# Performance work log

Measured on AMD Instinct MI355X. Metric: run time of the kernel, lower is better.

## Reference

```python
import jax, jax.numpy as jnp
import numpy as np

EMB_SIZE = 256  # VQ embedding_size
BETA = 0.25     # commitment cost


def _mlp(x, W1, b1, W2, b2, W3, b3):
    h = jax.nn.relu(x @ W1 + b1)
    h = jax.nn.relu(h @ W2 + b2)
    return h @ W3 + b3


def setup_inputs() -> dict:
    key = jax.random.key(0)
    ks = jax.random.split(key, 5)
    B, D = 1024, 1024
    s = 1.0 / np.sqrt(D)
    return {
        "observation": jax.random.normal(ks[0], (B, D), jnp.float32),
        "W1": jax.random.normal(ks[1], (D, D), jnp.float32) * s,
        "b1": jnp.zeros((D,), jnp.float32),
        "W2": jax.random.normal(ks[2], (D, D), jnp.float32) * s,
        "b2": jnp.zeros((D,), jnp.float32),
        "W3": jax.random.normal(ks[3], (D, D), jnp.float32) * s,
        "b3": jnp.zeros((D,), jnp.float32),
        "codebook": jax.random.normal(ks[4], (512, EMB_SIZE), jnp.float32),
    }


def reference(observation, W1, b1, W2, b2, W3, b3, codebook):
    # Dense encoder
    features = _mlp(observation, W1, b1, W2, b2, W3, b3)  # [B, 1024]
    # Flatten features into embedding_size-dim tokens: [B*4, 256]
    z = features.reshape(-1, EMB_SIZE)
    # Squared euclidean distances to codebook: [N, K]
    d = (jnp.sum(z * z, axis=1, keepdims=True)
         - 2.0 * (z @ codebook.T)
         + jnp.sum(codebook * codebook, axis=1)[None, :])
    idx = jnp.argmin(d, axis=1)                   # [N] nearest code indices
    quantized = codebook[idx]                     # [N, 256] gather
    # VQ losses
    commitment_loss = jnp.mean((jax.lax.stop_gradient(quantized) - z) ** 2)
    codebook_loss = jnp.mean((quantized - jax.lax.stop_gradient(z)) ** 2)
    loss = codebook_loss + BETA * commitment_loss
    # Straight-through estimator
    quantized_st = z + jax.lax.stop_gradient(quantized - z)
    out = quantized_st.reshape(features.shape)    # [B, 1024]
    return out, loss, idx
```

## Files before the change

### kernel.cpp

```cpp
#include <hip/hip_runtime.h>


typedef _Float16 half8 __attribute__((ext_vector_type(8)));
typedef _Float16 half4 __attribute__((ext_vector_type(4)));
typedef float floatx4 __attribute__((ext_vector_type(4)));

#define LO_SCALE 2048.0f
#define INV_LO_SCALE (1.0f / 2048.0f)

__device__ __forceinline__ int remap4(int k0)
{
    return (k0 & 32) | ((k0 & 12) << 1) | ((k0 & 16) >> 2);
}
__device__ __forceinline__ int remap1(int k)
{
    return (k & ~63) | (k & 32) | ((k & 12) << 1) | ((k & 16) >> 2) | (k & 3);
}

__device__ __forceinline__ void gl_lds16(const _Float16* g, _Float16* l)
{
    __builtin_amdgcn_global_load_lds(
        (const __attribute__((address_space(1))) void*)g,
        (__attribute__((address_space(3))) void*)l, 16, 0, 0);
}

__device__ __forceinline__ half8 rfrag(const _Float16* m, int row, int ks, int fg)
{
    const int ch = ((ks << 2) + fg) ^ (row & 7);
    return *reinterpret_cast<const half8*>(&m[(row << 6) + (ch << 3)]);
}

template <bool RELU, bool WF32, bool WSPLIT>
__global__ __launch_bounds__(256) void gemm_k(
    const _Float16* __restrict__ Ah, const _Float16* __restrict__ Al,
    const _Float16* __restrict__ Bh, const _Float16* __restrict__ Bl,
    const float* __restrict__ bias,
    float* __restrict__ Cf, _Float16* __restrict__ Ch, _Float16* __restrict__ Cl,
    int N, int K)
{
    __shared__ __align__(16) _Float16 sm[2][192 * 64];

    const int tid = threadIdx.x;
    const int m0 = blockIdx.y * 32, n0 = blockIdx.x * 64;
    const int w = tid >> 6, lane = tid & 63;
    const int srow = lane >> 3, sc = lane & 7;

    const int wm = (w & 1) * 16, wn = (w >> 1) * 32;
    const int fr = lane & 15, fg = lane >> 4;

    floatx4 hh[2] = {};
    floatx4 m1[2] = {};
    floatx4 m2[2] = {};

    const int NT = K >> 6;

    auto STAGE = [&](int buf, int t) {
        const int kb = t << 6;
        #pragma unroll
        for (int s = 0; s < 6; ++s) {
            const int task = w * 6 + s;
            const _Float16* gb;
            int grow, lrow;
            if (task < 4)       { gb = Ah; grow = m0 + task * 8;        lrow = task * 8; }
            else if (task < 8)  { gb = Al; grow = m0 + (task - 4) * 8;  lrow = 32 + (task - 4) * 8; }
            else if (task < 16) { gb = Bh; grow = n0 + (task - 8) * 8;  lrow = 64 + (task - 8) * 8; }
            else                { gb = Bl; grow = n0 + (task - 16) * 8; lrow = 128 + (task - 16) * 8; }
            const _Float16* g = gb + (size_t)(grow + srow) * K + kb + ((sc ^ srow) << 3);
            gl_lds16(g, &sm[buf][lrow << 6]);
        }
    };

    STAGE(0, 0);
    __syncthreads();

    for (int t = 0; t < NT; ++t) {
        const int cur = t & 1;
        if (t + 1 < NT) STAGE(cur ^ 1, t + 1);
        const _Float16* S0 = sm[cur];
        #pragma unroll
        for (int ks = 0; ks < 2; ++ks) {
            const half8 a_h  = rfrag(S0, wm + fr, ks, fg);
            const half8 a_l  = rfrag(S0, 32 + wm + fr, ks, fg);
            const half8 b_h0 = rfrag(S0, 64 + wn + fr, ks, fg);
            const half8 b_h1 = rfrag(S0, 64 + wn + 16 + fr, ks, fg);
            const half8 b_l0 = rfrag(S0, 128 + wn + fr, ks, fg);
            const half8 b_l1 = rfrag(S0, 128 + wn + 16 + fr, ks, fg);
            hh[0] = __builtin_amdgcn_mfma_f32_16x16x32_f16(a_h, b_h0, hh[0], 0, 0, 0);
            hh[1] = __builtin_amdgcn_mfma_f32_16x16x32_f16(a_h, b_h1, hh[1], 0, 0, 0);
            m1[0] = __builtin_amdgcn_mfma_f32_16x16x32_f16(a_h, b_l0, m1[0], 0, 0, 0);
            m1[1] = __builtin_amdgcn_mfma_f32_16x16x32_f16(a_h, b_l1, m1[1], 0, 0, 0);
            m2[0] = __builtin_amdgcn_mfma_f32_16x16x32_f16(a_l, b_h0, m2[0], 0, 0, 0);
            m2[1] = __builtin_amdgcn_mfma_f32_16x16x32_f16(a_l, b_h1, m2[1], 0, 0, 0);
        }
        __syncthreads();
    }

    #pragma unroll
    for (int j = 0; j < 2; ++j) {
        const int col = n0 + wn + j * 16 + fr;
        const float bv = bias ? bias[col] : 0.0f;
        const int colr = remap1(col);
        #pragma unroll
        for (int r = 0; r < 4; ++r) {
            const int row = m0 + wm + fg * 4 + r;
            float v = hh[j][r] + (m1[j][r] + m2[j][r]) * INV_LO_SCALE + bv;
            if (RELU) v = fmaxf(v, 0.0f);
            if (WF32) Cf[(size_t)row * N + col] = v;
            if (WSPLIT) {
                const size_t o = (size_t)row * N + colr;
                const _Float16 hi = (_Float16)v;
                Ch[o] = hi;
                Cl[o] = (_Float16)((v - (float)hi) * LO_SCALE);
            }
        }
    }
}

__global__ __launch_bounds__(256) void prep_kernel(
    const float* __restrict__ W1, const float* __restrict__ W2,
    const float* __restrict__ W3, const float* __restrict__ obs,
    const float* __restrict__ CB,
    _Float16* __restrict__ T1h, _Float16* __restrict__ T1l,
    _Float16* __restrict__ T2h, _Float16* __restrict__ T2l,
    _Float16* __restrict__ T3h, _Float16* __restrict__ T3l,
    _Float16* __restrict__ Oh, _Float16* __restrict__ Ol,
    _Float16* __restrict__ CBh, _Float16* __restrict__ CBl,
    float* __restrict__ cnorm)
{
    __shared__ float tile[64][65];
    const int b = blockIdx.x, tid = threadIdx.x;

    if (b < 768) {
        const int z = b >> 8, rem = b & 255;
        const float* Wm = (z == 0) ? W1 : (z == 1) ? W2 : W3;
        _Float16* Th = (z == 0) ? T1h : (z == 1) ? T2h : T3h;
        _Float16* Tl = (z == 0) ? T1l : (z == 1) ? T2l : T3l;
        const int nb = (rem & 15) * 64, kb = (rem >> 4) * 64;
        {
            const int kr = tid >> 2, c0 = (tid & 3) * 16;
            #pragma unroll
            for (int c = 0; c < 16; c += 4) {
                float4 v = *reinterpret_cast<const float4*>(
                    &Wm[(size_t)(kb + kr) * 1024 + nb + c0 + c]);
                tile[kr][c0 + c] = v.x; tile[kr][c0 + c + 1] = v.y;
                tile[kr][c0 + c + 2] = v.z; tile[kr][c0 + c + 3] = v.w;
            }
        }
        __syncthreads();
        {
            const int nr = tid >> 2, k0 = (tid & 3) * 16;
            #pragma unroll
            for (int g = 0; g < 4; ++g) {
                const int kk = k0 + g * 4;
                half4 h, lo;
                #pragma unroll
                for (int j = 0; j < 4; ++j) {
                    const float x = tile[kk + j][nr];
                    const _Float16 hi = (_Float16)x;
                    h[j] = hi;
                    lo[j] = (_Float16)((x - (float)hi) * LO_SCALE);
                }
                const size_t o = (size_t)(nb + nr) * 1024 + kb + remap4(kk);
                *reinterpret_cast<half4*>(&Th[o]) = h;
                *reinterpret_cast<half4*>(&Tl[o]) = lo;
            }
        }
    } else if (b < 1280) {
        const size_t e0 = ((size_t)(b - 768) * 256 + tid) * 8;
        float4 a = *reinterpret_cast<const float4*>(&obs[e0]);
        float4 c = *reinterpret_cast<const float4*>(&obs[e0 + 4]);
        float xs[8] = {a.x, a.y, a.z, a.w, c.x, c.y, c.z, c.w};
        half4 h[2], lo[2];
        #pragma unroll
        for (int q = 0; q < 2; ++q)
            #pragma unroll
            for (int j = 0; j < 4; ++j) {
                const float x = xs[q * 4 + j];
                const _Float16 hi = (_Float16)x;
                h[q][j] = hi;
                lo[q][j] = (_Float16)((x - (float)hi) * LO_SCALE);
            }
        const size_t base = e0 & ~(size_t)63;
        const int r1 = remap4((int)(e0 & 63));
        const int r2 = remap4((int)((e0 + 4) & 63));
        *reinterpret_cast<half4*>(&Oh[base + r1]) = h[0];
        *reinterpret_cast<half4*>(&Oh[base + r2]) = h[1];
        *reinterpret_cast<half4*>(&Ol[base + r1]) = lo[0];
        *reinterpret_cast<half4*>(&Ol[base + r2]) = lo[1];
    } else {
        const int wv = tid >> 6, lane = tid & 63;
        const int code = (b - 1280) * 4 + wv;
        const int k0 = lane * 4;
        float4 c = *reinterpret_cast<const float4*>(&CB[(size_t)code * 256 + k0]);
        float xs[4] = {c.x, c.y, c.z, c.w};
        half4 h, lo;
        float s = 0.f;
        #pragma unroll
        for (int j = 0; j < 4; ++j) {
            const _Float16 hi = (_Float16)xs[j];
            h[j] = hi;
            lo[j] = (_Float16)((xs[j] - (float)hi) * LO_SCALE);
            s += xs[j] * xs[j];
        }
        const size_t o = (size_t)code * 256 + (k0 & ~63) + remap4(k0 & 63);
        *reinterpret_cast<half4*>(&CBh[o]) = h;
        *reinterpret_cast<half4*>(&CBl[o]) = lo;
        #pragma unroll
        for (int off = 32; off; off >>= 1) s += __shfl_down(s, off);
        if (lane == 0) cnorm[code] = s;
    }
}

__global__ __launch_bounds__(512) void vq_kernel(
    const _Float16* __restrict__ Fh, const _Float16* __restrict__ Fl,
    const float* __restrict__ S, const float* __restrict__ CB,
    const float* __restrict__ cnorm,
    float* __restrict__ out, float* __restrict__ pl, float* __restrict__ idx_out)
{
    const int wid = threadIdx.x >> 6, lane = threadIdx.x & 63;
    const int n = blockIdx.x * 8 + wid;

    float best = 3.4e38f;
    int bidx = 0x7fffffff;
    #pragma unroll
    for (int j = 0; j < 8; ++j) {
        const int k = j * 64 + lane;
        const float v = fmaf(-2.0f, S[(size_t)n * 512 + k], cnorm[k]);
        if (v < best) { best = v; bidx = k; }
    }
    #pragma unroll
    for (int off = 32; off; off >>= 1) {
        const float ov = __shfl_down(best, off);
        const int oi = __shfl_down(bidx, off);
        if (ov < best || (ov == best && oi < bidx)) { best = ov; bidx = oi; }
    }
    bidx = __shfl(bidx, 0);
    best = __shfl(best, 0);

    const int base = n * 256 + lane * 4;
    half4 h4 = *reinterpret_cast<const half4*>(&Fh[base]);
    half4 l4 = *reinterpret_cast<const half4*>(&Fl[base]);
    float zn = 0.f;
    #pragma unroll
    for (int j = 0; j < 4; ++j) {
        const float z = (float)h4[j] + (float)l4[j] * INV_LO_SCALE;
        zn = fmaf(z, z, zn);
    }
    #pragma unroll
    for (int off = 32; off; off >>= 1) zn += __shfl_down(zn, off);

    float4 q4 = *reinterpret_cast<const float4*>(&CB[(size_t)bidx * 256 + lane * 4]);
    *reinterpret_cast<float4*>(&out[(size_t)n * 256 + lane * 4]) = q4;

    __shared__ float part[8];
    if (lane == 0) {
        part[wid] = zn + best;
        idx_out[n] = (float)bidx;
    }
    __syncthreads();
    if (threadIdx.x == 0) {
        float s = 0.f;
        #pragma unroll
        for (int i = 0; i < 8; ++i) s += part[i];
        pl[blockIdx.x] = s;
    }
}

__global__ __launch_bounds__(512) void finalize_kernel(
    const float* __restrict__ pl, float* __restrict__ loss_out)
{
    float s = pl[threadIdx.x];
    #pragma unroll
    for (int off = 32; off; off >>= 1) s += __shfl_down(s, off);
    __shared__ float p[8];
    if ((threadIdx.x & 63) == 0) p[threadIdx.x >> 6] = s;
    __syncthreads();
    if (threadIdx.x == 0) {
        float t = 0.f;
        #pragma unroll
        for (int i = 0; i < 8; ++i) t += p[i];
        loss_out[0] = 1.25f * t / 1048576.0f;
    }
}

extern "C" void kernel_launch(void* const* d_in, const int* in_sizes, int n_in,
                              void* d_out, int out_size, void* d_ws, size_t ws_size,
                              hipStream_t stream)
{
    const float* obs = (const float*)d_in[0];
    const float* W1  = (const float*)d_in[1];
    const float* b1  = (const float*)d_in[2];
    const float* W2  = (const float*)d_in[3];
    const float* b2  = (const float*)d_in[4];
    const float* W3  = (const float*)d_in[5];
    const float* b3  = (const float*)d_in[6];
    const float* CB  = (const float*)d_in[7];

    float* out = (float*)d_out;
    float* loss_out = out + 1048576;
    float* idx_out  = out + 1048577;

    char* Wp = (char*)d_ws;
    _Float16* Oh    = (_Float16*)(Wp + (0u  << 20));
    _Float16* Ol    = (_Float16*)(Wp + (2u  << 20));
    _Float16* W1t_h = (_Float16*)(Wp + (4u  << 20));
    _Float16* W1t_l = (_Float16*)(Wp + (6u  << 20));
    _Float16* W2t_h = (_Float16*)(Wp + (8u  << 20));
    _Float16* W2t_l = (_Float16*)(Wp + (10u << 20));
    _Float16* W3t_h = (_Float16*)(Wp + (12u << 20));
    _Float16* W3t_l = (_Float16*)(Wp + (14u << 20));
    _Float16* H1_h  = (_Float16*)(Wp + (16u << 20));
    _Float16* H1_l  = (_Float16*)(Wp + (18u << 20));
    _Float16* H2_h  = (_Float16*)(Wp + (20u << 20));
    _Float16* H2_l  = (_Float16*)(Wp + (22u << 20));
    _Float16* F_h   = (_Float16*)(Wp + (24u << 20));
    _Float16* F_l   = (_Float16*)(Wp + (26u << 20));
    float*    S     = (float*)(Wp + (28u << 20));
    _Float16* CB_h  = (_Float16*)(Wp + (36u << 20));
    _Float16* CB_l  = (_Float16*)(Wp + (36u << 20) + 512 * 256 * 2);
    float*    cn    = (float*)(Wp + (36u << 20) + 2 * 512 * 256 * 2);
    float*    pl    = cn + 512;

    prep_kernel<<<1408, 256, 0, stream>>>(
        W1, W2, W3, obs, CB,
        W1t_h, W1t_l, W2t_h, W2t_l, W3t_h, W3t_l,
        Oh, Ol, CB_h, CB_l, cn);

    gemm_k<true, false, true><<<dim3(16, 32), 256, 0, stream>>>(
        Oh, Ol, W1t_h, W1t_l, b1, nullptr, H1_h, H1_l, 1024, 1024);
    gemm_k<true, false, true><<<dim3(16, 32), 256, 0, stream>>>(
        H1_h, H1_l, W2t_h, W2t_l, b2, nullptr, H2_h, H2_l, 1024, 1024);
    gemm_k<false, false, true><<<dim3(16, 32), 256, 0, stream>>>(
        H2_h, H2_l, W3t_h, W3t_l, b3, nullptr, F_h, F_l, 1024, 1024);
    gemm_k<false, true, false><<<dim3(8, 128), 256, 0, stream>>>(
        F_h, F_l, CB_h, CB_l, nullptr, S, nullptr, nullptr, 512, 256);

    vq_kernel<<<512, 512, 0, stream>>>(F_h, F_l, S, CB, cn, out, pl, idx_out);
    finalize_kernel<<<1, 512, 0, stream>>>(pl, loss_out);
}
```

Baseline: 140.3 us.

## Enlarge GEMM tiles to 64x64 and fuse codebook argmin into distance GEMM

The GEMM block tile grows from 32x64 to 64x64, each wave computing a 32x32 sub-tile with 2x2 MFMA fragments, and staging is simplified so each wave loads one operand plane. The distance GEMM no longer writes the full fp32 score matrix; its epilogue computes per-row partial argmins over 64 codes and writes them to small buffers. The VQ kernel then reduces 8 partials per row instead of reading 512 scores. The aim is to raise MFMA work per LDS load and to cut global traffic for the score matrix. In exchange, GEMMs 1-3 launch half as many blocks (256 on a large GPU) and each thread holds more accumulator registers.

```diff
diff --git a/kernel.cpp b/kernel.cpp
--- a/kernel.cpp
+++ b/kernel.cpp
@@ -30,44 +30,41 @@
     return *reinterpret_cast<const half8*>(&m[(row << 6) + (ch << 3)]);
 }
 
-template <bool RELU, bool WF32, bool WSPLIT>
+template <bool RELU, bool WSPLIT, bool ARGMIN>
 __global__ __launch_bounds__(256) void gemm_k(
     const _Float16* __restrict__ Ah, const _Float16* __restrict__ Al,
     const _Float16* __restrict__ Bh, const _Float16* __restrict__ Bl,
     const float* __restrict__ bias,
-    float* __restrict__ Cf, _Float16* __restrict__ Ch, _Float16* __restrict__ Cl,
+    _Float16* __restrict__ Ch, _Float16* __restrict__ Cl,
+    const float* __restrict__ cnorm, float* __restrict__ pv, int* __restrict__ pi,
     int N, int K)
 {
-    __shared__ __align__(16) _Float16 sm[2][192 * 64];
+    __shared__ __align__(16) _Float16 sm[2][4][4096];
 
     const int tid = threadIdx.x;
-    const int m0 = blockIdx.y * 32, n0 = blockIdx.x * 64;
+    const int m0 = blockIdx.y * 64, n0 = blockIdx.x * 64;
     const int w = tid >> 6, lane = tid & 63;
     const int srow = lane >> 3, sc = lane & 7;
 
-    const int wm = (w & 1) * 16, wn = (w >> 1) * 32;
+    const _Float16* gsrc = (w == 0) ? Ah : (w == 1) ? Al : (w == 2) ? Bh : Bl;
+    const int rb0 = (w < 2) ? m0 : n0;
+    const size_t gbase = (size_t)(rb0 + srow) * K + ((sc ^ srow) << 3);
+
+    const int wm = (w & 1) * 32, wn = (w >> 1) * 32;
     const int fr = lane & 15, fg = lane >> 4;
 
-    floatx4 hh[2] = {};
-    floatx4 m1[2] = {};
-    floatx4 m2[2] = {};
+    floatx4 hh[2][2] = {};
+    floatx4 c1[2][2] = {};
+    floatx4 c2[2][2] = {};
 
     const int NT = K >> 6;
 
     auto STAGE = [&](int buf, int t) {
-        const int kb = t << 6;
-        #pragma unroll
-        for (int s = 0; s < 6; ++s) {
-            const int task = w * 6 + s;
-            const _Float16* gb;
-            int grow, lrow;
-            if (task < 4)       { gb = Ah; grow = m0 + task * 8;        lrow = task * 8; }
-            else if (task < 8)  { gb = Al; grow = m0 + (task - 4) * 8;  lrow = 32 + (task - 4) * 8; }
-            else if (task < 16) { gb = Bh; grow = n0 + (task - 8) * 8;  lrow = 64 + (task - 8) * 8; }
-            else                { gb = Bl; grow = n0 + (task - 16) * 8; lrow = 128 + (task - 16) * 8; }
-            const _Float16* g = gb + (size_t)(grow + srow) * K + kb + ((sc ^ srow) << 3);
-            gl_lds16(g, &sm[buf][lrow << 6]);
-        }
+        const size_t kb = (size_t)(t << 6);
+        #pragma unroll
+        for (int j = 0; j < 8; ++j)
+            gl_lds16(gsrc + gbase + (size_t)(j << 3) * K + kb,
+                     &sm[buf][w][(j << 3) << 6]);
     };
 
     STAGE(0, 0);
@@ -76,42 +73,85 @@
     for (int t = 0; t < NT; ++t) {
         const int cur = t & 1;
         if (t + 1 < NT) STAGE(cur ^ 1, t + 1);
-        const _Float16* S0 = sm[cur];
         #pragma unroll
         for (int ks = 0; ks < 2; ++ks) {
-            const half8 a_h  = rfrag(S0, wm + fr, ks, fg);
-            const half8 a_l  = rfrag(S0, 32 + wm + fr, ks, fg);
-            const half8 b_h0 = rfrag(S0, 64 + wn + fr, ks, fg);
-            const half8 b_h1 = rfrag(S0, 64 + wn + 16 + fr, ks, fg);
-            const half8 b_l0 = rfrag(S0, 128 + wn + fr, ks, fg);
-            const half8 b_l1 = rfrag(S0, 128 + wn + 16 + fr, ks, fg);
-            hh[0] = __builtin_amdgcn_mfma_f32_16x16x32_f16(a_h, b_h0, hh[0], 0, 0, 0);
-            hh[1] = __builtin_amdgcn_mfma_f32_16x16x32_f16(a_h, b_h1, hh[1], 0, 0, 0);
-            m1[0] = __builtin_amdgcn_mfma_f32_16x16x32_f16(a_h, b_l0, m1[0], 0, 0, 0);
-            m1[1] = __builtin_amdgcn_mfma_f32_16x16x32_f16(a_h, b_l1, m1[1], 0, 0, 0);
-            m2[0] = __builtin_amdgcn_mfma_f32_16x16x32_f16(a_l, b_h0, m2[0], 0, 0, 0);
-            m2[1] = __builtin_amdgcn_mfma_f32_16x16x32_f16(a_l, b_h1, m2[1], 0, 0, 0);
+            half8 a_h[2], a_l[2], b_h[2], b_l[2];
+            #pragma unroll
+            for (int i = 0; i < 2; ++i) {
+                a_h[i] = rfrag(sm[cur][0], wm + (i << 4) + fr, ks, fg);
+                a_l[i] = rfrag(sm[cur][1], wm + (i << 4) + fr, ks, fg);
+                b_h[i] = rfrag(sm[cur][2], wn + (i << 4) + fr, ks, fg);
+                b_l[i] = rfrag(sm[cur][3], wn + (i << 4) + fr, ks, fg);
+            }
+            #pragma unroll
+            for (int i = 0; i < 2; ++i)
+                #pragma unroll
+                for (int j = 0; j < 2; ++j) {
+                    hh[i][j] = __builtin_amdgcn_mfma_f32_16x16x32_f16(a_h[i], b_h[j], hh[i][j], 0, 0, 0);
+                    c1[i][j] = __builtin_amdgcn_mfma_f32_16x16x32_f16(a_h[i], b_l[j], c1[i][j], 0, 0, 0);
+                    c2[i][j] = __builtin_amdgcn_mfma_f32_16x16x32_f16(a_l[i], b_h[j], c2[i][j], 0, 0, 0);
+                }
         }
         __syncthreads();
     }
 
-    #pragma unroll
-    for (int j = 0; j < 2; ++j) {
-        const int col = n0 + wn + j * 16 + fr;
-        const float bv = bias ? bias[col] : 0.0f;
-        const int colr = remap1(col);
-        #pragma unroll
-        for (int r = 0; r < 4; ++r) {
-            const int row = m0 + wm + fg * 4 + r;
-            float v = hh[j][r] + (m1[j][r] + m2[j][r]) * INV_LO_SCALE + bv;
-            if (RELU) v = fmaxf(v, 0.0f);
-            if (WF32) Cf[(size_t)row * N + col] = v;
-            if (WSPLIT) {
-                const size_t o = (size_t)row * N + colr;
-                const _Float16 hi = (_Float16)v;
-                Ch[o] = hi;
-                Cl[o] = (_Float16)((v - (float)hi) * LO_SCALE);
-            }
+    if (!ARGMIN) {
+        #pragma unroll
+        for (int j = 0; j < 2; ++j) {
+            const int col = n0 + wn + (j << 4) + fr;
+            const float bv = bias ? bias[col] : 0.0f;
+            const int colr = remap1(col);
+            #pragma unroll
+            for (int i = 0; i < 2; ++i)
+                #pragma unroll
+                for (int r = 0; r < 4; ++r) {
+                    const int row = m0 + wm + (i << 4) + (fg << 2) + r;
+                    float v = hh[i][j][r] + (c1[i][j][r] + c2[i][j][r]) * INV_LO_SCALE + bv;
+                    if (RELU) v = fmaxf(v, 0.0f);
+                    if (WSPLIT) {
+                        const size_t o = (size_t)row * N + colr;
+                        const _Float16 hi = (_Float16)v;
+                        Ch[o] = hi;
+                        Cl[o] = (_Float16)((v - (float)hi) * LO_SCALE);
+                    }
+                }
+        }
+    } else {
+        const int cA = n0 + wn + fr, cB = cA + 16;
+        const float cnA = cnorm[cA], cnB = cnorm[cB];
+        float* cv = (float*)&sm[0][0][0];
+        int* ci = (int*)(cv + 128);
+        #pragma unroll
+        for (int i = 0; i < 2; ++i)
+            #pragma unroll
+            for (int r = 0; r < 4; ++r) {
+                const float v0 = hh[i][0][r] + (c1[i][0][r] + c2[i][0][r]) * INV_LO_SCALE;
+                const float v1 = hh[i][1][r] + (c1[i][1][r] + c2[i][1][r]) * INV_LO_SCALE;
+                const float d0 = fmaf(-2.0f, v0, cnA);
+                const float d1 = fmaf(-2.0f, v1, cnB);
+                float d = d0; int di = cA;
+                if (d1 < d0) { d = d1; di = cB; }
+                #pragma unroll
+                for (int msk = 1; msk <= 8; msk <<= 1) {
+                    const float ov = __shfl_xor(d, msk);
+                    const int oi = __shfl_xor(di, msk);
+                    if (ov < d || (ov == d && oi < di)) { d = ov; di = oi; }
+                }
+                if (fr == 0) {
+                    const int rl = (i << 4) + (fg << 2) + r;
+                    cv[w * 32 + rl] = d;
+                    ci[w * 32 + rl] = di;
+                }
+            }
+        __syncthreads();
+        if (tid < 64) {
+            const int a = tid >> 5, rl = tid & 31;
+            float d = cv[a * 32 + rl]; int di = ci[a * 32 + rl];
+            const float d2 = cv[(a + 2) * 32 + rl];
+            const int i2 = ci[(a + 2) * 32 + rl];
+            if (d2 < d || (d2 == d && i2 < di)) { d = d2; di = i2; }
+            pv[blockIdx.x * 4096 + m0 + tid] = d;
+            pi[blockIdx.x * 4096 + m0 + tid] = di;
         }
     }
 }
@@ -211,10 +251,10 @@
     }
 }
 
-__global__ __launch_bounds__(512) void vq_kernel(
+__global__ __launch_bounds__(512) void vq_lite_kernel(
+    const float* __restrict__ pv, const int* __restrict__ pi,
     const _Float16* __restrict__ Fh, const _Float16* __restrict__ Fl,
-    const float* __restrict__ S, const float* __restrict__ CB,
-    const float* __restrict__ cnorm,
+    const float* __restrict__ CB,
     float* __restrict__ out, float* __restrict__ pl, float* __restrict__ idx_out)
 {
     const int wid = threadIdx.x >> 6, lane = threadIdx.x & 63;
@@ -222,16 +262,11 @@
 
     float best = 3.4e38f;
     int bidx = 0x7fffffff;
+    if (lane < 8) { best = pv[lane * 4096 + n]; bidx = pi[lane * 4096 + n]; }
     #pragma unroll
-    for (int j = 0; j < 8; ++j) {
-        const int k = j * 64 + lane;
-        const float v = fmaf(-2.0f, S[(size_t)n * 512 + k], cnorm[k]);
-        if (v < best) { best = v; bidx = k; }
-    }
-    #pragma unroll
-    for (int off = 32; off; off >>= 1) {
-        const float ov = __shfl_down(best, off);
-        const int oi = __shfl_down(bidx, off);
+    for (int msk = 1; msk <= 4; msk <<= 1) {
+        const float ov = __shfl_xor(best, msk);
+        const int oi = __shfl_xor(bidx, msk);
         if (ov < best || (ov == best && oi < bidx)) { best = ov; bidx = oi; }
     }
     bidx = __shfl(bidx, 0);
@@ -315,26 +350,28 @@
     _Float16* H2_l  = (_Float16*)(Wp + (22u << 20));
     _Float16* F_h   = (_Float16*)(Wp + (24u << 20));
     _Float16* F_l   = (_Float16*)(Wp + (26u << 20));
-    float*    S     = (float*)(Wp + (28u << 20));
-    _Float16* CB_h  = (_Float16*)(Wp + (36u << 20));
-    _Float16* CB_l  = (_Float16*)(Wp + (36u << 20) + 512 * 256 * 2);
-    float*    cn    = (float*)(Wp + (36u << 20) + 2 * 512 * 256 * 2);
-    float*    pl    = cn + 512;
+    _Float16* CB_h  = (_Float16*)(Wp + (28u << 20));
+    _Float16* CB_l  = (_Float16*)(Wp + (28u << 20) + 512 * 256 * 2);
+    float*    cn    = (float*)(Wp + (28u << 20) + 2 * 512 * 256 * 2);
+    float*    pv    = (float*)(Wp + (29u << 20));
+    int*      pi    = (int*)(Wp + (30u << 20));
+    float*    pl    = (float*)(Wp + (31u << 20));
 
     prep_kernel<<<1408, 256, 0, stream>>>(
         W1, W2, W3, obs, CB,
         W1t_h, W1t_l, W2t_h, W2t_l, W3t_h, W3t_l,
         Oh, Ol, CB_h, CB_l, cn);
 
-    gemm_k<true, false, true><<<dim3(16, 32), 256, 0, stream>>>(
-        Oh, Ol, W1t_h, W1t_l, b1, nullptr, H1_h, H1_l, 1024, 1024);
-    gemm_k<true, false, true><<<dim3(16, 32), 256, 0, stream>>>(
-        H1_h, H1_l, W2t_h, W2t_l, b2, nullptr, H2_h, H2_l, 1024, 1024);
-    gemm_k<false, false, true><<<dim3(16, 32), 256, 0, stream>>>(
-        H2_h, H2_l, W3t_h, W3t_l, b3, nullptr, F_h, F_l, 1024, 1024);
-    gemm_k<false, true, false><<<dim3(8, 128), 256, 0, stream>>>(
-        F_h, F_l, CB_h, CB_l, nullptr, S, nullptr, nullptr, 512, 256);
-
-    vq_kernel<<<512, 512, 0, stream>>>(F_h, F_l, S, CB, cn, out, pl, idx_out);
+    gemm_k<true, true, false><<<dim3(16, 16), 256, 0, stream>>>(
+        Oh, Ol, W1t_h, W1t_l, b1, H1_h, H1_l, nullptr, nullptr, nullptr, 1024, 1024);
+    gemm_k<true, true, false><<<dim3(16, 16), 256, 0, stream>>>(
+        H1_h, H1_l, W2t_h, W2t_l, b2, H2_h, H2_l, nullptr, nullptr, nullptr, 1024, 1024);
+    gemm_k<false, true, false><<<dim3(16, 16), 256, 0, stream>>>(
+        H2_h, H2_l, W3t_h, W3t_l, b3, F_h, F_l, nullptr, nullptr, nullptr, 1024, 1024);
+
+    gemm_k<false, false, true><<<dim3(8, 64), 256, 0, stream>>>(
+        F_h, F_l, CB_h, CB_l, nullptr, nullptr, nullptr, cn, pv, pi, 512, 256);
+
+    vq_lite_kernel<<<512, 512, 0, stream>>>(pv, pi, F_h, F_l, CB, out, pl, idx_out);
     finalize_kernel<<<1, 512, 0, stream>>>(pl, loss_out);
 }
```

New measurement: 141.2 us. No clear change (+0.6%).
